# Optimization experiments

Hardware: AMD Instinct MI355X
Metric: run time of the kernel (lower is better)

Reference implementation:

```python
import jax, jax.numpy as jnp
import numpy as np

NS, NP, EJ, ER = 10000, 2048, 32768, 32768  # skills, job/resume pairs, edges
D, H = 1536, 8
NEG_SLOPE_ATT = 0.2   # GAT attention leaky_relu
NEG_SLOPE = 0.01      # F.leaky_relu / nn.LeakyReLU default


def setup_inputs() -> dict:
    key = jax.random.key(0)
    ks = jax.random.split(key, 20)
    rn = lambda k, shp, s=1.0: jax.random.normal(k, shp, dtype=jnp.float32) * s
    s_d = 1.0 / np.sqrt(D)
    return {
        "x_skill": rn(ks[0], (NS, D)),
        "x_job": rn(ks[1], (NP, D)),
        "x_resume": rn(ks[2], (NP, D)),
        # GraphConv params (lin_rel has bias, lin_root bias=False in PyG)
        "W_rel": rn(ks[3], (D, D), s_d),
        "b_rel": jnp.zeros((D,), jnp.float32),
        "W_root": rn(ks[4], (D, D), s_d),
        # GATConv params (heads=8, concat=False)
        "W_gat_src": rn(ks[5], (D, H * D), s_d),
        "W_gat_dst": rn(ks[6], (D, H * D), s_d),
        "att_src": rn(ks[7], (H, D), s_d),
        "att_dst": rn(ks[8], (H, D), s_d),
        "b_gat": jnp.zeros((D,), jnp.float32),
        # MLP: [3072 -> 512 -> 128 -> 1]
        "W1": rn(ks[9], (2 * D, 512), 1.0 / np.sqrt(2 * D)),
        "b1": jnp.zeros((512,), jnp.float32),
        "W2": rn(ks[10], (512, 128), 1.0 / np.sqrt(512)),
        "b2": jnp.zeros((128,), jnp.float32),
        "W3": rn(ks[11], (128, 1), 1.0 / np.sqrt(128)),
        "b3": jnp.zeros((1,), jnp.float32),
        # edge lists (src = skill idx, dst = job/resume idx)
        "edge_src_job": jax.random.randint(ks[12], (EJ,), 0, NS, dtype=jnp.int32),
        "edge_dst_job": jax.random.randint(ks[13], (EJ,), 0, NP, dtype=jnp.int32),
        "edge_src_res": jax.random.randint(ks[14], (ER,), 0, NS, dtype=jnp.int32),
        "edge_dst_res": jax.random.randint(ks[15], (ER,), 0, NP, dtype=jnp.int32),
    }


def reference(x_skill, x_job, x_resume, W_rel, b_rel, W_root,
              W_gat_src, W_gat_dst, att_src, att_dst, b_gat,
              W1, b1, W2, b2, W3, b3,
              edge_src_job, edge_dst_job, edge_src_res, edge_dst_res):
    n_pair = x_job.shape[0]

    # --- GraphConv (skill -> job): sum-aggregate then linear + root ---
    agg = jax.ops.segment_sum(x_skill[edge_src_job], edge_dst_job,
                              num_segments=n_pair)                  # [NP, D]
    h_job = agg @ W_rel + b_rel + x_job @ W_root                     # [NP, D]

    # --- GATConv (skill -> resume), heads=H, concat=False, no self-loops ---
    xs = (x_skill @ W_gat_src).reshape(-1, H, D)                     # [NS, H, D]
    xd = (x_resume @ W_gat_dst).reshape(-1, H, D)                    # [NP, H, D]
    a_src = jnp.einsum('nhd,hd->nh', xs, att_src)                    # [NS, H]
    a_dst = jnp.einsum('nhd,hd->nh', xd, att_dst)                    # [NP, H]
    e = jax.nn.leaky_relu(a_src[edge_src_res] + a_dst[edge_dst_res],
                          NEG_SLOPE_ATT)                             # [E, H]
    # segment softmax over edges grouped by destination resume node
    e_max = jax.ops.segment_max(e, edge_dst_res, num_segments=n_pair)
    e_exp = jnp.exp(e - e_max[edge_dst_res])
    denom = jax.ops.segment_sum(e_exp, edge_dst_res, num_segments=n_pair)
    alpha = e_exp / (denom[edge_dst_res] + 1e-16)                    # [E, H]
    msg = xs[edge_src_res] * alpha[:, :, None]                       # [E, H, D]
    out = jax.ops.segment_sum(msg, edge_dst_res, num_segments=n_pair)  # [NP, H, D]
    h_res = out.mean(axis=1) + b_gat                                 # concat=False -> head mean

    # --- combine + MLP ---
    h = jnp.concatenate([jax.nn.leaky_relu(h_job, NEG_SLOPE),
                         jax.nn.leaky_relu(h_res, NEG_SLOPE)], axis=1)  # [NP, 2D]
    h = jax.nn.leaky_relu(h @ W1 + b1, NEG_SLOPE)
    h = jax.nn.leaky_relu(h @ W2 + b2, NEG_SLOPE)
    score = (h @ W3 + b3).squeeze(-1)                                # [NP]
    return score, alpha
```

## Files before the change

kernel.cpp:

```cpp
#include <hip/hip_runtime.h>

#define D_ 1536
#define H_ 8

typedef __attribute__((ext_vector_type(8))) short bf16x8;
typedef __attribute__((ext_vector_type(4))) float f32x4;

__device__ __forceinline__ unsigned short f2bf(float f) {
    unsigned u = __builtin_bit_cast(unsigned, f);
    unsigned r = (u + 0x7fffu + ((u >> 16) & 1u)) >> 16;
    return (unsigned short)r;
}

__device__ __forceinline__ unsigned pack2bf(float a, float b) {
    return (unsigned)f2bf(a) | ((unsigned)f2bf(b) << 16);
}

__device__ __forceinline__ void gload16(const void* g, void* l) {
    __builtin_amdgcn_global_load_lds((const __attribute__((address_space(1))) void*)g,
                                     (__attribute__((address_space(3))) void*)l, 16, 0, 0);
}

__global__ __launch_bounds__(256) void k_vmat(const float* __restrict__ Wsrc,
                                              const float* __restrict__ Wdst,
                                              const float* __restrict__ att_s,
                                              const float* __restrict__ att_d,
                                              float* __restrict__ Vsrc,
                                              float* __restrict__ Vdst) {
    int id = blockIdx.x;
    int sel = id >= (D_ * H_);
    int idx = sel ? id - D_ * H_ : id;
    int d = idx >> 3, h = idx & 7;
    const float* W = (sel ? Wdst : Wsrc) + (size_t)d * (H_ * D_) + (size_t)h * D_;
    const float* at = (sel ? att_d : att_s) + (size_t)h * D_;
    float s = 0.f;
    for (int i = threadIdx.x; i < D_; i += 256) s += W[i] * at[i];
    for (int o = 32; o; o >>= 1) s += __shfl_down(s, o);
    __shared__ float red[4];
    if ((threadIdx.x & 63) == 0) red[threadIdx.x >> 6] = s;
    __syncthreads();
    if (threadIdx.x == 0) (sel ? Vdst : Vsrc)[d * H_ + h] = red[0] + red[1] + red[2] + red[3];
}

__global__ __launch_bounds__(256) void k_a(const float* __restrict__ x,
                                           const float* __restrict__ V,
                                           float* __restrict__ out, int N) {
    int n = blockIdx.x;
    if (n >= N) return;
    float part[H_] = {};
    const float* xr = x + (size_t)n * D_;
    #pragma unroll
    for (int j = 0; j < 6; j++) {
        int d = threadIdx.x + j * 256;
        float xv = xr[d];
        const float* vp = V + d * H_;
        #pragma unroll
        for (int h = 0; h < H_; h++) part[h] += xv * vp[h];
    }
    __shared__ float red[4][H_];
    int lane = threadIdx.x & 63, w = threadIdx.x >> 6;
    #pragma unroll
    for (int h = 0; h < H_; h++) {
        float v = part[h];
        for (int o = 32; o; o >>= 1) v += __shfl_down(v, o);
        if (lane == 0) red[w][h] = v;
    }
    __syncthreads();
    if (threadIdx.x < H_)
        out[(size_t)n * H_ + threadIdx.x] =
            red[0][threadIdx.x] + red[1][threadIdx.x] + red[2][threadIdx.x] + red[3][threadIdx.x];
}

__global__ void k_count(const int* __restrict__ dj, int ej, const int* __restrict__ dr, int er,
                        int* cnt_j, int* cnt_r) {
    int i = blockIdx.x * blockDim.x + threadIdx.x;
    if (i < ej) atomicAdd(&cnt_j[dj[i]], 1);
    else if (i < ej + er) atomicAdd(&cnt_r[dr[i - ej]], 1);
}

__global__ void k_scan(const int* __restrict__ cnt_j, int* off_j,
                       const int* __restrict__ cnt_r, int* off_r, int NP) {
    const int* cnt = blockIdx.x ? cnt_r : cnt_j;
    int* off = blockIdx.x ? off_r : off_j;
    int lane = threadIdx.x;
    int chunk = (NP + 63) / 64;
    int base = lane * chunk;
    int sum = 0;
    for (int i = 0; i < chunk; i++) { int idx = base + i; if (idx < NP) sum += cnt[idx]; }
    int incl = sum;
    for (int o = 1; o < 64; o <<= 1) { int t = __shfl_up(incl, o); if (lane >= o) incl += t; }
    int run = incl - sum;
    for (int i = 0; i < chunk; i++) { int idx = base + i; if (idx < NP) { off[idx] = run; run += cnt[idx]; } }
    if (lane == 63) off[NP] = run;
}

__global__ void k_scatter(const int* __restrict__ dj, int ej, const int* __restrict__ dr, int er,
                          const int* __restrict__ off_j, int* fill_j, int* sid_j,
                          const int* __restrict__ off_r, int* fill_r, int* sid_r) {
    int i = blockIdx.x * blockDim.x + threadIdx.x;
    if (i < ej) {
        int p = dj[i];
        int slot = atomicAdd(&fill_j[p], 1);
        sid_j[off_j[p] + slot] = i;
    } else if (i < ej + er) {
        int e = i - ej;
        int p = dr[e];
        int slot = atomicAdd(&fill_r[p], 1);
        sid_r[off_r[p] + slot] = e;
    }
}

__global__ __launch_bounds__(256) void k_agg(const float* __restrict__ x, const int* __restrict__ src,
                                             const int* __restrict__ sid, const int* __restrict__ cnt,
                                             const int* __restrict__ off, unsigned* __restrict__ cat_u) {
    int p = blockIdx.x;
    int n = cnt[p], o = off[p];
    const float2* x2 = (const float2*)x;
    float2 acc[3] = {};
    int i = 0;
    for (; i + 2 <= n; i += 2) {
        int e0 = sid[o + i], e1 = sid[o + i + 1];
        const float2* r0 = x2 + (size_t)src[e0] * 768 + threadIdx.x;
        const float2* r1 = x2 + (size_t)src[e1] * 768 + threadIdx.x;
        float2 v0[3], v1[3];
        #pragma unroll
        for (int j = 0; j < 3; j++) { v0[j] = r0[j * 256]; v1[j] = r1[j * 256]; }
        #pragma unroll
        for (int j = 0; j < 3; j++) {
            acc[j].x += v0[j].x + v1[j].x;
            acc[j].y += v0[j].y + v1[j].y;
        }
    }
    if (i < n) {
        int e0 = sid[o + i];
        const float2* r0 = x2 + (size_t)src[e0] * 768 + threadIdx.x;
        #pragma unroll
        for (int j = 0; j < 3; j++) { float2 v = r0[j * 256]; acc[j].x += v.x; acc[j].y += v.y; }
    }
    unsigned* orow = cat_u + (size_t)p * 1536 + threadIdx.x;
    #pragma unroll
    for (int j = 0; j < 3; j++) orow[j * 256] = pack2bf(acc[j].x, acc[j].y);
}

__global__ __launch_bounds__(256) void k_xjob(const float* __restrict__ x_job,
                                              unsigned* __restrict__ cat_u) {
    int p = blockIdx.x;
    const float2* xr = (const float2*)x_job + (size_t)p * 768 + threadIdx.x;
    unsigned* orow = cat_u + (size_t)p * 1536 + 768 + threadIdx.x;
    #pragma unroll
    for (int j = 0; j < 3; j++) { float2 v = xr[j * 256]; orow[j * 256] = pack2bf(v.x, v.y); }
}

__global__ void k_softmax(const float* __restrict__ a_src, const float* __restrict__ a_dst,
                          const int* __restrict__ src, const int* __restrict__ sid,
                          const int* __restrict__ cnt, const int* __restrict__ off,
                          float* __restrict__ alpha_out) {
    int p = blockIdx.x;
    int n = cnt[p], o = off[p];
    if (n == 0) return;
    int lane = threadIdx.x;
    #pragma unroll 1
    for (int h = 0; h < H_; h++) {
        float ad = a_dst[(size_t)p * H_ + h];
        float m = -3.4e38f;
        for (int i = lane; i < n; i += 64) {
            int e = sid[o + i];
            float v = a_src[(size_t)src[e] * H_ + h] + ad;
            v = v >= 0.f ? v : 0.2f * v;
            m = fmaxf(m, v);
        }
        for (int o2 = 32; o2; o2 >>= 1) m = fmaxf(m, __shfl_xor(m, o2));
        float s = 0.f;
        for (int i = lane; i < n; i += 64) {
            int e = sid[o + i];
            float v = a_src[(size_t)src[e] * H_ + h] + ad;
            v = v >= 0.f ? v : 0.2f * v;
            s += expf(v - m);
        }
        for (int o2 = 32; o2; o2 >>= 1) s += __shfl_xor(s, o2);
        float inv = 1.f / (s + 1e-16f);
        for (int i = lane; i < n; i += 64) {
            int e = sid[o + i];
            float v = a_src[(size_t)src[e] * H_ + h] + ad;
            v = v >= 0.f ? v : 0.2f * v;
            alpha_out[(size_t)e * H_ + h] = expf(v - m) * inv;
        }
    }
}

__global__ __launch_bounds__(256) void k_aggatt(const float* __restrict__ x,
                                                const float* __restrict__ alpha,
                                                const int* __restrict__ src, const int* __restrict__ sid,
                                                const int* __restrict__ cnt, const int* __restrict__ off,
                                                unsigned* __restrict__ aggatt_u) {
    int p = blockIdx.x;
    int n = cnt[p], o = off[p];
    const float2* x2 = (const float2*)x;
    float2 acc[H_][3] = {};
    int i = 0;
    for (; i + 2 <= n; i += 2) {
        int e0 = sid[o + i], e1 = sid[o + i + 1];
        const float2* r0 = x2 + (size_t)src[e0] * 768 + threadIdx.x;
        const float2* r1 = x2 + (size_t)src[e1] * 768 + threadIdx.x;
        float2 v0[3], v1[3];
        #pragma unroll
        for (int j = 0; j < 3; j++) { v0[j] = r0[j * 256]; v1[j] = r1[j * 256]; }
        const float* a0 = alpha + (size_t)e0 * H_;
        const float* a1 = alpha + (size_t)e1 * H_;
        #pragma unroll
        for (int h = 0; h < H_; h++) {
            float w0 = a0[h], w1 = a1[h];
            #pragma unroll
            for (int j = 0; j < 3; j++) {
                acc[h][j].x += w0 * v0[j].x + w1 * v1[j].x;
                acc[h][j].y += w0 * v0[j].y + w1 * v1[j].y;
            }
        }
    }
    if (i < n) {
        int e0 = sid[o + i];
        const float2* r0 = x2 + (size_t)src[e0] * 768 + threadIdx.x;
        float2 v0[3];
        #pragma unroll
        for (int j = 0; j < 3; j++) v0[j] = r0[j * 256];
        const float* a0 = alpha + (size_t)e0 * H_;
        #pragma unroll
        for (int h = 0; h < H_; h++) {
            float w0 = a0[h];
            #pragma unroll
            for (int j = 0; j < 3; j++) { acc[h][j].x += w0 * v0[j].x; acc[h][j].y += w0 * v0[j].y; }
        }
    }
    unsigned* orow = aggatt_u + (size_t)p * (H_ * 768) + threadIdx.x;
    #pragma unroll
    for (int h = 0; h < H_; h++)
        #pragma unroll
        for (int j = 0; j < 3; j++)
            orow[h * 768 + j * 256] = pack2bf(acc[h][j].x, acc[h][j].y);
}

template <int GATB>
__global__ __launch_bounds__(256) void k_tr(const float* __restrict__ in, int ldin,
                                            unsigned short* __restrict__ out, int ldout) {
    __shared__ float t[64][65];
    int k0 = blockIdx.y * 64, n0 = blockIdx.x * 64;
    int tx = threadIdx.x & 63, ty = threadIdx.x >> 6;
    #pragma unroll
    for (int i = 0; i < 16; i++) {
        int k = k0 + ty + i * 4;
        const float* rp;
        if (GATB) {
            int d2 = k % D_, h = k / D_;
            rp = in + (size_t)d2 * (H_ * D_) + (size_t)h * D_;
        } else {
            rp = in + (size_t)k * ldin;
        }
        t[ty + i * 4][tx] = rp[n0 + tx];
    }
    __syncthreads();
    #pragma unroll
    for (int i = 0; i < 16; i++) {
        int n = n0 + ty + i * 4;
        out[(size_t)n * ldout + k0 + tx] = f2bf(t[tx][ty + i * 4]);
    }
}

__global__ __launch_bounds__(256) void gemm_sk2(const unsigned short* __restrict__ A, int lda,
                                                const unsigned short* __restrict__ BT, int ldb,
                                                float* __restrict__ P, int N, int Kc) {
    __shared__ unsigned short As[2][128 * 32];
    __shared__ unsigned short Bs[2][128 * 32];
    int tid = threadIdx.x;
    int lane = tid & 63, wid = tid >> 6;

    int nwg = gridDim.x * gridDim.y;
    int bidh = blockIdx.y * gridDim.x + blockIdx.x;
    int swz = (bidh & 7) * (nwg >> 3) + (bidh >> 3);
    int bn = (swz % gridDim.x) * 128;
    int bm = (swz / gridDim.x) * 128;

    int kbase = blockIdx.z * Kc, kend = kbase + Kc;
    int wr = wid >> 1, wc = wid & 1;
    int fr = lane & 15, g = lane >> 4;
    int srow = lane >> 2, ssl = lane & 3;

    f32x4 acc[4][4] = {};

    auto stage = [&](int buf, int k0) {
        #pragma unroll
        for (int i = 0; i < 2; i++) {
            int c = wid * 2 + i;
            int r = c * 16 + srow;
            int sg = ssl ^ ((r >> 1) & 3);
            gload16(A + (size_t)(bm + r) * lda + k0 + sg * 8, &As[buf][c * 512]);
            gload16(BT + (size_t)(bn + r) * ldb + k0 + sg * 8, &Bs[buf][c * 512]);
        }
    };

    stage(0, kbase);
    int cur = 0;
    for (int k0 = kbase; k0 < kend; k0 += 32) {
        if (k0 + 32 < kend) {
            stage(cur ^ 1, k0 + 32);
            asm volatile("s_waitcnt vmcnt(4)" ::: "memory");
        } else {
            asm volatile("s_waitcnt vmcnt(0)" ::: "memory");
        }
        __builtin_amdgcn_s_barrier();
        __builtin_amdgcn_sched_barrier(0);
        bf16x8 a[4], b[4];
        #pragma unroll
        for (int mi = 0; mi < 4; mi++) {
            int row = wr * 64 + mi * 16 + fr;
            a[mi] = *(const bf16x8*)(&As[cur][row * 32 + ((g ^ ((row >> 1) & 3)) * 8)]);
        }
        #pragma unroll
        for (int ni = 0; ni < 4; ni++) {
            int row = wc * 64 + ni * 16 + fr;
            b[ni] = *(const bf16x8*)(&Bs[cur][row * 32 + ((g ^ ((row >> 1) & 3)) * 8)]);
        }
        __builtin_amdgcn_s_setprio(1);
        #pragma unroll
        for (int mi = 0; mi < 4; mi++)
            #pragma unroll
            for (int ni = 0; ni < 4; ni++)
                acc[mi][ni] = __builtin_amdgcn_mfma_f32_16x16x32_bf16(a[mi], b[ni], acc[mi][ni], 0, 0, 0);
        __builtin_amdgcn_s_setprio(0);
        __builtin_amdgcn_s_barrier();
        __builtin_amdgcn_sched_barrier(0);
        cur ^= 1;
    }

    size_t MN = (size_t)N * (size_t)(gridDim.y * 128);
    float* Pz = P + (size_t)blockIdx.z * MN;
    #pragma unroll
    for (int mi = 0; mi < 4; mi++) {
        int r0 = bm + wr * 64 + mi * 16 + (lane >> 4) * 4;
        #pragma unroll
        for (int ni = 0; ni < 4; ni++) {
            int c = bn + wc * 64 + ni * 16 + (lane & 15);
            #pragma unroll
            for (int j = 0; j < 4; j++)
                Pz[(size_t)(r0 + j) * N + c] = acc[mi][ni][j];
        }
    }
}

template <int OUT_BF16>
__global__ __launch_bounds__(256) void k_reduce(const float* __restrict__ P, int S, int MN, int N,
                                                void* __restrict__ Cout, int ldc,
                                                const float* __restrict__ bias, float scale,
                                                int useLeaky) {
    int idx = (blockIdx.x * 256 + threadIdx.x) * 4;
    if (idx >= MN) return;
    float4 v = *(const float4*)(P + idx);
    for (int s = 1; s < S; s++) {
        float4 t = *(const float4*)(P + (size_t)s * MN + idx);
        v.x += t.x; v.y += t.y; v.z += t.z; v.w += t.w;
    }
    int m = idx / N, n = idx - m * N;
    float vv[4] = {v.x, v.y, v.z, v.w};
    #pragma unroll
    for (int j = 0; j < 4; j++) {
        float x = vv[j] * scale + bias[n + j];
        if (useLeaky) x = x >= 0.f ? x : 0.01f * x;
        if (OUT_BF16) ((unsigned short*)Cout)[(size_t)m * ldc + n + j] = f2bf(x);
        else ((float*)Cout)[(size_t)m * ldc + n + j] = x;
    }
}

__global__ void k_score(const float* __restrict__ h2, const float* __restrict__ W3,
                        const float* __restrict__ b3, float* __restrict__ out) {
    int p = blockIdx.x;
    int lane = threadIdx.x;
    const float* r = h2 + (size_t)p * 128;
    float s = r[lane] * W3[lane] + r[lane + 64] * W3[lane + 64];
    for (int o = 32; o; o >>= 1) s += __shfl_down(s, o);
    if (lane == 0) out[p] = s + b3[0];
}

extern "C" void kernel_launch(void* const* d_in, const int* in_sizes, int n_in,
                              void* d_out, int out_size, void* d_ws, size_t ws_size,
                              hipStream_t stream) {
    const float* x_skill = (const float*)d_in[0];
    const float* x_job   = (const float*)d_in[1];
    const float* x_resume= (const float*)d_in[2];
    const float* W_rel   = (const float*)d_in[3];
    const float* b_rel   = (const float*)d_in[4];
    const float* W_root  = (const float*)d_in[5];
    const float* W_gs    = (const float*)d_in[6];
    const float* W_gd    = (const float*)d_in[7];
    const float* att_s   = (const float*)d_in[8];
    const float* att_d   = (const float*)d_in[9];
    const float* b_gat   = (const float*)d_in[10];
    const float* W1      = (const float*)d_in[11];
    const float* b1      = (const float*)d_in[12];
    const float* W2      = (const float*)d_in[13];
    const float* b2      = (const float*)d_in[14];
    const float* W3      = (const float*)d_in[15];
    const float* b3      = (const float*)d_in[16];
    const int* esj = (const int*)d_in[17];
    const int* edj = (const int*)d_in[18];
    const int* esr = (const int*)d_in[19];
    const int* edr = (const int*)d_in[20];

    const int NS = in_sizes[0] / D_;
    const int NP = in_sizes[1] / D_;
    const int EJ = in_sizes[17];
    const int ER = in_sizes[19];

    float* score = (float*)d_out;
    float* alpha = score + NP;

    char* ws = (char*)d_ws;
    size_t off = 0;
    auto alloc = [&](size_t bytes) -> void* {
        void* p = ws + off;
        off = (off + bytes + 255) & ~(size_t)255;
        return p;
    };

    int* cnt_j  = (int*)alloc((size_t)4 * NP * sizeof(int));
    int* fill_j = cnt_j + NP;
    int* cnt_r  = cnt_j + 2 * NP;
    int* fill_r = cnt_j + 3 * NP;
    int* off_j  = (int*)alloc((size_t)(NP + 1) * sizeof(int));
    int* off_r  = (int*)alloc((size_t)(NP + 1) * sizeof(int));
    int* sid_j  = (int*)alloc((size_t)EJ * sizeof(int));
    int* sid_r  = (int*)alloc((size_t)ER * sizeof(int));
    float* Vsrc = (float*)alloc((size_t)D_ * H_ * 4);
    float* Vdst = (float*)alloc((size_t)D_ * H_ * 4);
    float* a_src= (float*)alloc((size_t)NS * H_ * 4);
    float* a_dst= (float*)alloc((size_t)NP * H_ * 4);
    unsigned short* cat_in = (unsigned short*)alloc((size_t)NP * 2 * D_ * 2);
    unsigned short* aggatt = (unsigned short*)alloc((size_t)NP * H_ * D_ * 2);
    unsigned short* BT1    = (unsigned short*)alloc((size_t)D_ * 2 * D_ * 2);
    unsigned short* BTg    = (unsigned short*)alloc((size_t)D_ * H_ * D_ * 2);
    unsigned short* BTw1   = (unsigned short*)alloc((size_t)512 * 2 * D_ * 2);
    unsigned short* BTw2   = (unsigned short*)alloc((size_t)128 * 512 * 2);
    unsigned short* hcat   = (unsigned short*)alloc((size_t)NP * 2 * D_ * 2);
    unsigned short* h1b    = (unsigned short*)alloc((size_t)NP * 512 * 2);
    float* h2   = (float*)alloc((size_t)NP * 128 * 4);
    float* Pbuf = (float*)alloc((size_t)4 * NP * D_ * 4);

    hipMemsetAsync(cnt_j, 0, (size_t)4 * NP * sizeof(int), stream);

    k_tr<0><<<dim3(D_ / 64, D_ / 64), 256, 0, stream>>>(W_rel, D_, BT1, 2 * D_);
    k_tr<0><<<dim3(D_ / 64, D_ / 64), 256, 0, stream>>>(W_root, D_, BT1 + D_, 2 * D_);
    k_tr<1><<<dim3(D_ / 64, (H_ * D_) / 64), 256, 0, stream>>>(W_gs, 0, BTg, H_ * D_);
    k_tr<0><<<dim3(512 / 64, (2 * D_) / 64), 256, 0, stream>>>(W1, 512, BTw1, 2 * D_);
    k_tr<0><<<dim3(128 / 64, 512 / 64), 256, 0, stream>>>(W2, 128, BTw2, 512);

    k_vmat<<<2 * D_ * H_, 256, 0, stream>>>(W_gs, W_gd, att_s, att_d, Vsrc, Vdst);
    k_a<<<NS, 256, 0, stream>>>(x_skill, Vsrc, a_src, NS);
    k_a<<<NP, 256, 0, stream>>>(x_resume, Vdst, a_dst, NP);

    int egrid = (EJ + ER + 255) / 256;
    k_count<<<egrid, 256, 0, stream>>>(edj, EJ, edr, ER, cnt_j, cnt_r);
    k_scan<<<2, 64, 0, stream>>>(cnt_j, off_j, cnt_r, off_r, NP);
    k_scatter<<<egrid, 256, 0, stream>>>(edj, EJ, edr, ER, off_j, fill_j, sid_j, off_r, fill_r, sid_r);

    k_agg<<<NP, 256, 0, stream>>>(x_skill, esj, sid_j, cnt_j, off_j, (unsigned*)cat_in);
    k_xjob<<<NP, 256, 0, stream>>>(x_job, (unsigned*)cat_in);
    k_softmax<<<NP, 64, 0, stream>>>(a_src, a_dst, esr, sid_r, cnt_r, off_r, alpha);
    k_aggatt<<<NP, 256, 0, stream>>>(x_skill, alpha, esr, sid_r, cnt_r, off_r, (unsigned*)aggatt);

    const int MN_f = NP * D_;
    const int MN_1 = NP * 512;
    const int MN_2 = NP * 128;

    gemm_sk2<<<dim3(D_ / 128, NP / 128, 4), 256, 0, stream>>>(
        cat_in, 2 * D_, BT1, 2 * D_, Pbuf, D_, 768);
    k_reduce<1><<<MN_f / 1024, 256, 0, stream>>>(Pbuf, 4, MN_f, D_, hcat, 2 * D_, b_rel, 1.f, 1);

    gemm_sk2<<<dim3(D_ / 128, NP / 128, 4), 256, 0, stream>>>(
        aggatt, H_ * D_, BTg, H_ * D_, Pbuf, D_, 3072);
    k_reduce<1><<<MN_f / 1024, 256, 0, stream>>>(Pbuf, 4, MN_f, D_, hcat + D_, 2 * D_, b_gat, 1.f / H_, 1);

    gemm_sk2<<<dim3(512 / 128, NP / 128, 8), 256, 0, stream>>>(
        hcat, 2 * D_, BTw1, 2 * D_, Pbuf, 512, 384);
    k_reduce<1><<<MN_1 / 1024, 256, 0, stream>>>(Pbuf, 8, MN_1, 512, h1b, 512, b1, 1.f, 1);

    gemm_sk2<<<dim3(128 / 128, NP / 128, 4), 256, 0, stream>>>(
        h1b, 512, BTw2, 512, Pbuf, 128, 128);
    k_reduce<0><<<MN_2 / 1024, 256, 0, stream>>>(Pbuf, 4, MN_2, 128, h2, 128, b2, 1.f, 1);

    k_score<<<NP, 64, 0, stream>>>(h2, W3, b3, score);
}
```

Before: 452.9 us.

## Gather bf16 skill rows, enlarge GEMM tiles to 256x128, rebalance split-K

Converts x_skill to bf16 once and has both neighbour aggregation kernels gather the half-size rows, which cuts gather bandwidth. The split-K GEMM is replaced by a 512-thread kernel with 256x128 tiles and uneven split-K partitions (5 or 16 splits), so the block counts fit the CU count better. The weight-transpose kernel now writes packed bf16 pairs. Risks include extra rounding on the aggregation inputs and wider partial-sum buffers for the reduce kernels.

Measured after the change: 452.1 us. About the same (-0.2%).

```diff
diff --git a/kernel.cpp b/kernel.cpp
--- a/kernel.cpp
+++ b/kernel.cpp
@@ -15,6 +15,9 @@
 __device__ __forceinline__ unsigned pack2bf(float a, float b) {
     return (unsigned)f2bf(a) | ((unsigned)f2bf(b) << 16);
 }
+
+__device__ __forceinline__ float bflo(unsigned u) { return __builtin_bit_cast(float, u << 16); }
+__device__ __forceinline__ float bfhi(unsigned u) { return __builtin_bit_cast(float, u & 0xffff0000u); }
 
 __device__ __forceinline__ void gload16(const void* g, void* l) {
     __builtin_amdgcn_global_load_lds((const __attribute__((address_space(1))) void*)g,
@@ -110,32 +113,39 @@
     }
 }
 
-__global__ __launch_bounds__(256) void k_agg(const float* __restrict__ x, const int* __restrict__ src,
+__global__ __launch_bounds__(256) void k_xsb(const float* __restrict__ x, unsigned* __restrict__ xb) {
+    int p = blockIdx.x;
+    const float2* xr = (const float2*)x + (size_t)p * 768 + threadIdx.x;
+    unsigned* o = xb + (size_t)p * 768 + threadIdx.x;
+    #pragma unroll
+    for (int j = 0; j < 3; j++) { float2 v = xr[j * 256]; o[j * 256] = pack2bf(v.x, v.y); }
+}
+
+__global__ __launch_bounds__(256) void k_agg(const unsigned* __restrict__ xb, const int* __restrict__ src,
                                              const int* __restrict__ sid, const int* __restrict__ cnt,
                                              const int* __restrict__ off, unsigned* __restrict__ cat_u) {
     int p = blockIdx.x;
     int n = cnt[p], o = off[p];
-    const float2* x2 = (const float2*)x;
     float2 acc[3] = {};
     int i = 0;
     for (; i + 2 <= n; i += 2) {
         int e0 = sid[o + i], e1 = sid[o + i + 1];
-        const float2* r0 = x2 + (size_t)src[e0] * 768 + threadIdx.x;
-        const float2* r1 = x2 + (size_t)src[e1] * 768 + threadIdx.x;
-        float2 v0[3], v1[3];
+        const unsigned* r0 = xb + (size_t)src[e0] * 768 + threadIdx.x;
+        const unsigned* r1 = xb + (size_t)src[e1] * 768 + threadIdx.x;
+        unsigned v0[3], v1[3];
         #pragma unroll
         for (int j = 0; j < 3; j++) { v0[j] = r0[j * 256]; v1[j] = r1[j * 256]; }
         #pragma unroll
         for (int j = 0; j < 3; j++) {
-            acc[j].x += v0[j].x + v1[j].x;
-            acc[j].y += v0[j].y + v1[j].y;
+            acc[j].x += bflo(v0[j]) + bflo(v1[j]);
+            acc[j].y += bfhi(v0[j]) + bfhi(v1[j]);
         }
     }
     if (i < n) {
         int e0 = sid[o + i];
-        const float2* r0 = x2 + (size_t)src[e0] * 768 + threadIdx.x;
-        #pragma unroll
-        for (int j = 0; j < 3; j++) { float2 v = r0[j * 256]; acc[j].x += v.x; acc[j].y += v.y; }
+        const unsigned* r0 = xb + (size_t)src[e0] * 768 + threadIdx.x;
+        #pragma unroll
+        for (int j = 0; j < 3; j++) { unsigned v = r0[j * 256]; acc[j].x += bflo(v); acc[j].y += bfhi(v); }
     }
     unsigned* orow = cat_u + (size_t)p * 1536 + threadIdx.x;
     #pragma unroll
@@ -188,39 +198,44 @@
     }
 }
 
-__global__ __launch_bounds__(256) void k_aggatt(const float* __restrict__ x,
+__global__ __launch_bounds__(256) void k_aggatt(const unsigned* __restrict__ xb,
                                                 const float* __restrict__ alpha,
                                                 const int* __restrict__ src, const int* __restrict__ sid,
                                                 const int* __restrict__ cnt, const int* __restrict__ off,
                                                 unsigned* __restrict__ aggatt_u) {
     int p = blockIdx.x;
     int n = cnt[p], o = off[p];
-    const float2* x2 = (const float2*)x;
     float2 acc[H_][3] = {};
     int i = 0;
     for (; i + 2 <= n; i += 2) {
         int e0 = sid[o + i], e1 = sid[o + i + 1];
-        const float2* r0 = x2 + (size_t)src[e0] * 768 + threadIdx.x;
-        const float2* r1 = x2 + (size_t)src[e1] * 768 + threadIdx.x;
-        float2 v0[3], v1[3];
+        const unsigned* r0 = xb + (size_t)src[e0] * 768 + threadIdx.x;
+        const unsigned* r1 = xb + (size_t)src[e1] * 768 + threadIdx.x;
+        unsigned v0[3], v1[3];
         #pragma unroll
         for (int j = 0; j < 3; j++) { v0[j] = r0[j * 256]; v1[j] = r1[j * 256]; }
         const float* a0 = alpha + (size_t)e0 * H_;
         const float* a1 = alpha + (size_t)e1 * H_;
+        float f0[3][2], f1[3][2];
+        #pragma unroll
+        for (int j = 0; j < 3; j++) {
+            f0[j][0] = bflo(v0[j]); f0[j][1] = bfhi(v0[j]);
+            f1[j][0] = bflo(v1[j]); f1[j][1] = bfhi(v1[j]);
+        }
         #pragma unroll
         for (int h = 0; h < H_; h++) {
             float w0 = a0[h], w1 = a1[h];
             #pragma unroll
             for (int j = 0; j < 3; j++) {
-                acc[h][j].x += w0 * v0[j].x + w1 * v1[j].x;
-                acc[h][j].y += w0 * v0[j].y + w1 * v1[j].y;
+                acc[h][j].x += w0 * f0[j][0] + w1 * f1[j][0];
+                acc[h][j].y += w0 * f0[j][1] + w1 * f1[j][1];
             }
         }
     }
     if (i < n) {
         int e0 = sid[o + i];
-        const float2* r0 = x2 + (size_t)src[e0] * 768 + threadIdx.x;
-        float2 v0[3];
+        const unsigned* r0 = xb + (size_t)src[e0] * 768 + threadIdx.x;
+        unsigned v0[3];
         #pragma unroll
         for (int j = 0; j < 3; j++) v0[j] = r0[j * 256];
         const float* a0 = alpha + (size_t)e0 * H_;
@@ -228,7 +243,10 @@
         for (int h = 0; h < H_; h++) {
             float w0 = a0[h];
             #pragma unroll
-            for (int j = 0; j < 3; j++) { acc[h][j].x += w0 * v0[j].x; acc[h][j].y += w0 * v0[j].y; }
+            for (int j = 0; j < 3; j++) {
+                acc[h][j].x += w0 * bflo(v0[j]);
+                acc[h][j].y += w0 * bfhi(v0[j]);
+            }
         }
     }
     unsigned* orow = aggatt_u + (size_t)p * (H_ * 768) + threadIdx.x;
@@ -258,17 +276,19 @@
         t[ty + i * 4][tx] = rp[n0 + tx];
     }
     __syncthreads();
-    #pragma unroll
-    for (int i = 0; i < 16; i++) {
-        int n = n0 + ty + i * 4;
-        out[(size_t)n * ldout + k0 + tx] = f2bf(t[tx][ty + i * 4]);
-    }
-}
-
-__global__ __launch_bounds__(256) void gemm_sk2(const unsigned short* __restrict__ A, int lda,
-                                                const unsigned short* __restrict__ BT, int ldb,
-                                                float* __restrict__ P, int N, int Kc) {
-    __shared__ unsigned short As[2][128 * 32];
+    int tx2 = threadIdx.x & 31, ty2 = threadIdx.x >> 5;
+    #pragma unroll
+    for (int i = 0; i < 8; i++) {
+        int nl = ty2 + i * 8;
+        unsigned v = pack2bf(t[tx2 * 2][nl], t[tx2 * 2 + 1][nl]);
+        *(unsigned*)(out + (size_t)(n0 + nl) * ldout + k0 + tx2 * 2) = v;
+    }
+}
+
+__global__ __launch_bounds__(512, 4) void gemm_sk(const unsigned short* __restrict__ A, int lda,
+                                                  const unsigned short* __restrict__ BT, int ldb,
+                                                  float* __restrict__ P, int N, int bs, int extra) {
+    __shared__ unsigned short As[2][256 * 32];
     __shared__ unsigned short Bs[2][128 * 32];
     int tid = threadIdx.x;
     int lane = tid & 63, wid = tid >> 6;
@@ -277,24 +297,28 @@
     int bidh = blockIdx.y * gridDim.x + blockIdx.x;
     int swz = (bidh & 7) * (nwg >> 3) + (bidh >> 3);
     int bn = (swz % gridDim.x) * 128;
-    int bm = (swz / gridDim.x) * 128;
-
-    int kbase = blockIdx.z * Kc, kend = kbase + Kc;
+    int bm = (swz / gridDim.x) * 256;
+
+    int z = blockIdx.z;
+    int steps = bs + (z < extra);
+    int kb = z * bs + min(z, extra);
+    int kbase = kb * 32, kend = kbase + steps * 32;
+
     int wr = wid >> 1, wc = wid & 1;
     int fr = lane & 15, g = lane >> 4;
-    int srow = lane >> 2, ssl = lane & 3;
+
+    int ra0 = tid >> 2, sa0 = tid & 3;
+    int ra1 = (tid + 512) >> 2, sa1 = tid & 3;
+    int sg_a0 = sa0 ^ ((ra0 >> 1) & 3);
+    int sg_a1 = sa1 ^ ((ra1 >> 1) & 3);
+    int sg_b = sa0 ^ ((ra0 >> 1) & 3);
 
     f32x4 acc[4][4] = {};
 
     auto stage = [&](int buf, int k0) {
-        #pragma unroll
-        for (int i = 0; i < 2; i++) {
-            int c = wid * 2 + i;
-            int r = c * 16 + srow;
-            int sg = ssl ^ ((r >> 1) & 3);
-            gload16(A + (size_t)(bm + r) * lda + k0 + sg * 8, &As[buf][c * 512]);
-            gload16(BT + (size_t)(bn + r) * ldb + k0 + sg * 8, &Bs[buf][c * 512]);
-        }
+        gload16(A + (size_t)(bm + ra0) * lda + k0 + sg_a0 * 8, &As[buf][tid * 8]);
+        gload16(A + (size_t)(bm + ra1) * lda + k0 + sg_a1 * 8, &As[buf][(tid + 512) * 8]);
+        gload16(BT + (size_t)(bn + ra0) * ldb + k0 + sg_b * 8, &Bs[buf][tid * 8]);
     };
 
     stage(0, kbase);
@@ -302,7 +326,7 @@
     for (int k0 = kbase; k0 < kend; k0 += 32) {
         if (k0 + 32 < kend) {
             stage(cur ^ 1, k0 + 32);
-            asm volatile("s_waitcnt vmcnt(4)" ::: "memory");
+            asm volatile("s_waitcnt vmcnt(3)" ::: "memory");
         } else {
             asm volatile("s_waitcnt vmcnt(0)" ::: "memory");
         }
@@ -331,8 +355,8 @@
         cur ^= 1;
     }
 
-    size_t MN = (size_t)N * (size_t)(gridDim.y * 128);
-    float* Pz = P + (size_t)blockIdx.z * MN;
+    size_t MN = (size_t)N * (size_t)(gridDim.y * 256);
+    float* Pz = P + (size_t)z * MN;
     #pragma unroll
     for (int mi = 0; mi < 4; mi++) {
         int r0 = bm + wr * 64 + mi * 16 + (lane >> 4) * 4;
@@ -441,7 +465,8 @@
     unsigned short* hcat   = (unsigned short*)alloc((size_t)NP * 2 * D_ * 2);
     unsigned short* h1b    = (unsigned short*)alloc((size_t)NP * 512 * 2);
     float* h2   = (float*)alloc((size_t)NP * 128 * 4);
-    float* Pbuf = (float*)alloc((size_t)4 * NP * D_ * 4);
+    float* Pbuf = (float*)alloc((size_t)16 * NP * 512 * 4);
+    unsigned* xsb = (unsigned*)Pbuf;
 
     hipMemsetAsync(cnt_j, 0, (size_t)4 * NP * sizeof(int), stream);
 
@@ -451,6 +476,7 @@
     k_tr<0><<<dim3(512 / 64, (2 * D_) / 64), 256, 0, stream>>>(W1, 512, BTw1, 2 * D_);
     k_tr<0><<<dim3(128 / 64, 512 / 64), 256, 0, stream>>>(W2, 128, BTw2, 512);
 
+    k_xsb<<<NS, 256, 0, stream>>>(x_skill, xsb);
     k_vmat<<<2 * D_ * H_, 256, 0, stream>>>(W_gs, W_gd, att_s, att_d, Vsrc, Vdst);
     k_a<<<NS, 256, 0, stream>>>(x_skill, Vsrc, a_src, NS);
     k_a<<<NP, 256, 0, stream>>>(x_resume, Vdst, a_dst, NP);
@@ -460,30 +486,30 @@
     k_scan<<<2, 64, 0, stream>>>(cnt_j, off_j, cnt_r, off_r, NP);
     k_scatter<<<egrid, 256, 0, stream>>>(edj, EJ, edr, ER, off_j, fill_j, sid_j, off_r, fill_r, sid_r);
 
-    k_agg<<<NP, 256, 0, stream>>>(x_skill, esj, sid_j, cnt_j, off_j, (unsigned*)cat_in);
+    k_agg<<<NP, 256, 0, stream>>>(xsb, esj, sid_j, cnt_j, off_j, (unsigned*)cat_in);
     k_xjob<<<NP, 256, 0, stream>>>(x_job, (unsigned*)cat_in);
     k_softmax<<<NP, 64, 0, stream>>>(a_src, a_dst, esr, sid_r, cnt_r, off_r, alpha);
-    k_aggatt<<<NP, 256, 0, stream>>>(x_skill, alpha, esr, sid_r, cnt_r, off_r, (unsigned*)aggatt);
+    k_aggatt<<<NP, 256, 0, stream>>>(xsb, alpha, esr, sid_r, cnt_r, off_r, (unsigned*)aggatt);
 
     const int MN_f = NP * D_;
     const int MN_1 = NP * 512;
     const int MN_2 = NP * 128;
 
-    gemm_sk2<<<dim3(D_ / 128, NP / 128, 4), 256, 0, stream>>>(
-        cat_in, 2 * D_, BT1, 2 * D_, Pbuf, D_, 768);
-    k_reduce<1><<<MN_f / 1024, 256, 0, stream>>>(Pbuf, 4, MN_f, D_, hcat, 2 * D_, b_rel, 1.f, 1);
-
-    gemm_sk2<<<dim3(D_ / 128, NP / 128, 4), 256, 0, stream>>>(
-        aggatt, H_ * D_, BTg, H_ * D_, Pbuf, D_, 3072);
-    k_reduce<1><<<MN_f / 1024, 256, 0, stream>>>(Pbuf, 4, MN_f, D_, hcat + D_, 2 * D_, b_gat, 1.f / H_, 1);
-
-    gemm_sk2<<<dim3(512 / 128, NP / 128, 8), 256, 0, stream>>>(
-        hcat, 2 * D_, BTw1, 2 * D_, Pbuf, 512, 384);
-    k_reduce<1><<<MN_1 / 1024, 256, 0, stream>>>(Pbuf, 8, MN_1, 512, h1b, 512, b1, 1.f, 1);
-
-    gemm_sk2<<<dim3(128 / 128, NP / 128, 4), 256, 0, stream>>>(
-        h1b, 512, BTw2, 512, Pbuf, 128, 128);
-    k_reduce<0><<<MN_2 / 1024, 256, 0, stream>>>(Pbuf, 4, MN_2, 128, h2, 128, b2, 1.f, 1);
+    gemm_sk<<<dim3(D_ / 128, NP / 256, 5), 512, 0, stream>>>(
+        cat_in, 2 * D_, BT1, 2 * D_, Pbuf, D_, 19, 1);
+    k_reduce<1><<<MN_f / 1024, 256, 0, stream>>>(Pbuf, 5, MN_f, D_, hcat, 2 * D_, b_rel, 1.f, 1);
+
+    gemm_sk<<<dim3(D_ / 128, NP / 256, 5), 512, 0, stream>>>(
+        aggatt, H_ * D_, BTg, H_ * D_, Pbuf, D_, 76, 4);
+    k_reduce<1><<<MN_f / 1024, 256, 0, stream>>>(Pbuf, 5, MN_f, D_, hcat + D_, 2 * D_, b_gat, 1.f / H_, 1);
+
+    gemm_sk<<<dim3(512 / 128, NP / 256, 16), 512, 0, stream>>>(
+        hcat, 2 * D_, BTw1, 2 * D_, Pbuf, 512, 6, 0);
+    k_reduce<1><<<MN_1 / 1024, 256, 0, stream>>>(Pbuf, 16, MN_1, 512, h1b, 512, b1, 1.f, 1);
+
+    gemm_sk<<<dim3(128 / 128, NP / 256, 16), 512, 0, stream>>>(
+        h1b, 512, BTw2, 512, Pbuf, 128, 1, 0);
+    k_reduce<0><<<MN_2 / 1024, 256, 0, stream>>>(Pbuf, 16, MN_2, 128, h2, 128, b2, 1.f, 1);
 
     k_score<<<NP, 64, 0, stream>>>(h2, W3, b3, score);
 }
```
